# Optimization experiments

Hardware: AMD Instinct MI355X
Metric: run time of the kernel (lower is better)

The kernel has to match this reference:

```python
import jax, jax.numpy as jnp
import numpy as np
import math

HEAD_DIM = 128
DEPTH = 12
LAMBDA_INIT = 0.8 - 0.6 * math.exp(-0.3 * DEPTH)
EPS = 1e-5
SCALE = 1.0 / math.sqrt(HEAD_DIM / 2)


def setup_inputs() -> dict:
    key = jax.random.key(0)
    ks = jax.random.split(key, 8)
    b, t, d = 2, 4096, 2048
    return {
        "x": jax.random.normal(ks[0], (b, t, d), dtype=jnp.float32),
        "wq": jax.random.normal(ks[1], (d, HEAD_DIM), dtype=jnp.float32) * 0.02,
        "wk": jax.random.normal(ks[2], (d, HEAD_DIM), dtype=jnp.float32) * 0.02,
        "wv": jax.random.normal(ks[3], (d, HEAD_DIM), dtype=jnp.float32) * 0.02,
        "lambda_q1": jax.random.normal(ks[4], (HEAD_DIM // 2,), dtype=jnp.float32) * 0.1,
        "lambda_q2": jax.random.normal(ks[5], (HEAD_DIM // 2,), dtype=jnp.float32) * 0.1,
        "lambda_k1": jax.random.normal(ks[6], (HEAD_DIM // 2,), dtype=jnp.float32) * 0.1,
        "lambda_k2": jax.random.normal(ks[7], (HEAD_DIM // 2,), dtype=jnp.float32) * 0.1,
        "ln_weight": jnp.ones((HEAD_DIM,), dtype=jnp.float32),
    }


def reference(x, wq, wk, wv, lambda_q1, lambda_q2, lambda_k1, lambda_k2, ln_weight):
    b, t, d = x.shape
    q = x @ wq  # [b,t,hd]
    k = x @ wk
    v = x @ wv
    h = HEAD_DIM // 2
    q1, q2 = q[..., :h], q[..., h:]
    k1, k2 = k[..., :h], k[..., h:]
    # causal mask: True where attention is disallowed (strictly upper triangle)
    causal = jnp.triu(jnp.ones((t, t), dtype=bool), k=1)
    neg_inf = jnp.float32(-jnp.inf)

    def masked_softmax(qh, kh):
        scores = jnp.einsum('btd,bsd->bts', qh, kh) * SCALE
        scores = jnp.where(causal, neg_inf, scores)
        return jax.nn.softmax(scores, axis=-1)

    a1 = masked_softmax(q1, k1)
    a2 = masked_softmax(q2, k2)
    lmbda = (jnp.exp(jnp.sum(lambda_q1 * lambda_k1))
             - jnp.exp(jnp.sum(lambda_q2 * lambda_k2))
             + LAMBDA_INIT)
    diffattn = jnp.einsum('bts,bsd->btd', a1 - lmbda * a2, v)
    rms = jnp.sqrt(jnp.mean(diffattn * diffattn, axis=-1, keepdims=True) + EPS)
    out = (1.0 - LAMBDA_INIT) * (diffattn / rms * ln_weight)
    return out
```

## Files before the change

kernel.cpp:

```cpp
#include <hip/hip_runtime.h>
#include <stdint.h>

#define T_SEQ 4096
#define NB 2
#define D_MODEL 2048
#define HD 128

typedef __attribute__((ext_vector_type(4)))  float f32x4;
typedef __attribute__((ext_vector_type(16))) float f32x16;
typedef __attribute__((ext_vector_type(8)))  short bf16x8;
typedef __attribute__((ext_vector_type(4)))  unsigned u32x4;

#define LAMBDA_INIT 0.7836057665316244f
#define OUT_SCALE   0.21639423346837556f

__device__ __forceinline__ unsigned short f2bf(float f) {
  unsigned int u = __float_as_uint(f);
  u += 0x7FFFu + ((u >> 16) & 1u);
  return (unsigned short)(u >> 16);
}
__device__ __forceinline__ float bf2f(unsigned short h) {
  return __uint_as_float(((unsigned int)h) << 16);
}
__device__ __forceinline__ unsigned cvt_pk_bf16(float a, float b) {
  unsigned r;
  asm("v_cvt_pk_bf16_f32 %0, %1, %2" : "=v"(r) : "v"(a), "v"(b));
  return r;
}
__device__ __forceinline__ void gload16(const void* g, void* l) {
  __builtin_amdgcn_global_load_lds(
      (const __attribute__((address_space(1))) unsigned int*)g,
      (__attribute__((address_space(3))) unsigned int*)l, 16, 0, 0);
}

__global__ __launch_bounds__(256) void wtrans(
    const float* __restrict__ wq, const float* __restrict__ wk,
    const float* __restrict__ wv, unsigned short* __restrict__ wT)
{
  const int which = blockIdx.y;
  const int s = blockIdx.x;
  const float* w = (which == 0) ? wq : ((which == 1) ? wk : wv);
  const float scale = (which == 0) ? 0.125f : 1.0f;
  const int tid = threadIdx.x;
  #pragma unroll
  for (int j = 0; j < 4; ++j) {
    int cell = j * 256 + tid;
    int q = cell >> 7, n = cell & 127;
    int kb = s * 64 + q * 8;
    float v[8];
    #pragma unroll
    for (int e = 0; e < 8; ++e) v[e] = w[(size_t)(kb + e) * HD + n] * scale;
    u32x4 pk = { cvt_pk_bf16(v[0], v[1]), cvt_pk_bf16(v[2], v[3]),
                 cvt_pk_bf16(v[4], v[5]), cvt_pk_bf16(v[6], v[7]) };
    *reinterpret_cast<u32x4*>(&wT[(size_t)(which * 32 + s) * 8192 + (size_t)cell * 8]) = pk;
  }
}

__global__ __launch_bounds__(256, 2) void qkv_proj(
    const float* __restrict__ x, const unsigned short* __restrict__ wT,
    unsigned short* __restrict__ qb, unsigned short* __restrict__ kS,
    unsigned short* __restrict__ vS)
{
  __shared__ __align__(16) unsigned short Ab[2][4096];
  __shared__ __align__(16) unsigned short Bb[2][8192];
  const int which = blockIdx.y;
  const int m0 = blockIdx.x * 64;
  const int tid = threadIdx.x;
  const int lane = tid & 63, wid = tid >> 6;
  const int wm = wid >> 1, wn = wid & 1;
  const int fr = lane & 15, fq = lane >> 4;

  const unsigned short* wslab = wT + (size_t)which * 32 * 8192;

  const int arow = tid & 31, aq = tid >> 5;
  const float* xa = x + (size_t)(m0 + arow) * D_MODEL + aq * 8;
  const float* xb = xa + (size_t)32 * D_MODEL;

  f32x4 acc[2][4];
  #pragma unroll
  for (int i = 0; i < 2; ++i)
    #pragma unroll
    for (int j = 0; j < 4; ++j) acc[i][j] = (f32x4){0.f, 0.f, 0.f, 0.f};

  {
    f32x4 u0 = *reinterpret_cast<const f32x4*>(xa);
    f32x4 u1 = *reinterpret_cast<const f32x4*>(xa + 4);
    f32x4 u2 = *reinterpret_cast<const f32x4*>(xb);
    f32x4 u3 = *reinterpret_cast<const f32x4*>(xb + 4);
    u32x4 c0 = { cvt_pk_bf16(u0[0], u0[1]), cvt_pk_bf16(u0[2], u0[3]),
                 cvt_pk_bf16(u1[0], u1[1]), cvt_pk_bf16(u1[2], u1[3]) };
    u32x4 c1 = { cvt_pk_bf16(u2[0], u2[1]), cvt_pk_bf16(u2[2], u2[3]),
                 cvt_pk_bf16(u3[0], u3[1]), cvt_pk_bf16(u3[2], u3[3]) };
    *reinterpret_cast<u32x4*>(&Ab[0][(size_t)(aq * 64 + arow) * 8]) = c0;
    *reinterpret_cast<u32x4*>(&Ab[0][(size_t)(aq * 64 + arow + 32) * 8]) = c1;
    #pragma unroll
    for (int j = 0; j < 4; ++j) {
      int ch = wid * 4 + j;
      gload16(wslab + (size_t)ch * 512 + (size_t)lane * 8, (char*)&Bb[0][ch * 512]);
    }
  }
  f32x4 a0 = *reinterpret_cast<const f32x4*>(xa + 64);
  f32x4 a1 = *reinterpret_cast<const f32x4*>(xa + 68);
  f32x4 a2 = *reinterpret_cast<const f32x4*>(xb + 64);
  f32x4 a3 = *reinterpret_cast<const f32x4*>(xb + 68);
  __syncthreads();

  for (int it = 0; it < 32; ++it) {
    const int cur = it & 1;
    if (it < 31) {
      #pragma unroll
      for (int j = 0; j < 4; ++j) {
        int ch = wid * 4 + j;
        gload16(wslab + (size_t)(it + 1) * 8192 + (size_t)ch * 512 + (size_t)lane * 8,
                (char*)&Bb[cur ^ 1][ch * 512]);
      }
      u32x4 c0 = { cvt_pk_bf16(a0[0], a0[1]), cvt_pk_bf16(a0[2], a0[3]),
                   cvt_pk_bf16(a1[0], a1[1]), cvt_pk_bf16(a1[2], a1[3]) };
      u32x4 c1 = { cvt_pk_bf16(a2[0], a2[1]), cvt_pk_bf16(a2[2], a2[3]),
                   cvt_pk_bf16(a3[0], a3[1]), cvt_pk_bf16(a3[2], a3[3]) };
      *reinterpret_cast<u32x4*>(&Ab[cur ^ 1][(size_t)(aq * 64 + arow) * 8]) = c0;
      *reinterpret_cast<u32x4*>(&Ab[cur ^ 1][(size_t)(aq * 64 + arow + 32) * 8]) = c1;
      if (it < 30) {
        const int kn = (it + 2) * 64;
        a0 = *reinterpret_cast<const f32x4*>(xa + kn);
        a1 = *reinterpret_cast<const f32x4*>(xa + kn + 4);
        a2 = *reinterpret_cast<const f32x4*>(xb + kn);
        a3 = *reinterpret_cast<const f32x4*>(xb + kn + 4);
      }
    }
    bf16x8 ah[2][2], bh[2][4];
    #pragma unroll
    for (int mi = 0; mi < 2; ++mi) {
      int row = wm * 32 + mi * 16 + fr;
      ah[mi][0] = *reinterpret_cast<bf16x8*>(&Ab[cur][(size_t)(fq * 64 + row) * 8]);
      ah[mi][1] = *reinterpret_cast<bf16x8*>(&Ab[cur][(size_t)((4 + fq) * 64 + row) * 8]);
    }
    #pragma unroll
    for (int ni = 0; ni < 4; ++ni) {
      int nrow = wn * 64 + ni * 16 + fr;
      bh[0][ni] = *reinterpret_cast<bf16x8*>(&Bb[cur][(size_t)(fq * 128 + nrow) * 8]);
      bh[1][ni] = *reinterpret_cast<bf16x8*>(&Bb[cur][(size_t)((4 + fq) * 128 + nrow) * 8]);
    }
    #pragma unroll
    for (int kk = 0; kk < 2; ++kk)
      #pragma unroll
      for (int mi = 0; mi < 2; ++mi)
        #pragma unroll
        for (int ni = 0; ni < 4; ++ni)
          acc[mi][ni] = __builtin_amdgcn_mfma_f32_16x16x32_bf16(ah[mi][kk], bh[kk][ni], acc[mi][ni], 0, 0, 0);
    __syncthreads();
  }
  #pragma unroll
  for (int mi = 0; mi < 2; ++mi)
    #pragma unroll
    for (int ni = 0; ni < 4; ++ni) {
      int n = wn * 64 + ni * 16 + fr;
      #pragma unroll
      for (int r = 0; r < 4; ++r) {
        int m = m0 + wm * 32 + mi * 16 + fq * 4 + r;
        float vv = acc[mi][ni][r];
        int bb = m >> 12, tt = m & 4095;
        int kt = tt >> 5, kvl = tt & 31;
        if (which == 0) {
          qb[(size_t)m * HD + n] = f2bf(vv);
        } else if (which == 1) {
          int g = n >> 6, hl = n & 63;
          int ks = hl >> 4, r8 = (hl >> 3) & 1, e = hl & 7;
          size_t idx = ((((((size_t)bb * 128 + kt) * 2 + g) * 4) + ks) << 9)
                     + (size_t)(kvl + 32 * r8) * 8 + e;
          kS[idx] = f2bf(vv);
        } else {
          int f = kvl >> 4, r8 = (kvl >> 3) & 1, e = kvl & 7;
          int vcb = n >> 5;
          size_t idx = (((((size_t)bb * 128 + kt) * 8) + vcb * 2 + f) << 9)
                     + (size_t)((n & 31) + 32 * r8) * 8 + e;
          vS[idx] = f2bf(vv);
        }
      }
    }
}

template<int LOG2S>
__global__ __launch_bounds__(256, 2) void diff_attn_part(
    const unsigned short* __restrict__ qb, const unsigned short* __restrict__ kS,
    const unsigned short* __restrict__ vS,
    unsigned short* __restrict__ po, float* __restrict__ pm, float* __restrict__ pl)
{
  constexpr int S = 1 << LOG2S;
  const int tid = threadIdx.x, lane = tid & 63, wid = tid >> 6;
  const int wave_id = blockIdx.x * 4 + wid;
  const int sp = wave_id & (S - 1);
  const int g  = (wave_id >> LOG2S) & 1;
  const int qt_raw = (wave_id >> (LOG2S + 1)) & 127;
  const int b  = wave_id >> (LOG2S + 8);
  const int qt = 127 - qt_raw;
  const int slot = (((b * 128 + qt) * 2 + g) << LOG2S) + sp;
  const int lq = lane & 31, lh = lane >> 5;
  const int q0 = qt * 32;
  const int n  = qt + 1;
  const int kt0 = (n * sp) >> LOG2S;
  const int kt1 = (n * (sp + 1)) >> LOG2S;

  bf16x8 qf[4];
  const unsigned short* qp = qb + ((size_t)b * T_SEQ + q0 + lq) * HD + g * 64 + lh * 8;
  #pragma unroll
  for (int ks = 0; ks < 4; ++ks) qf[ks] = *reinterpret_cast<const bf16x8*>(qp + ks * 16);

  f32x16 acc[4];
  #pragma unroll
  for (int v = 0; v < 4; ++v)
    #pragma unroll
    for (int r = 0; r < 16; ++r) acc[v][r] = 0.f;
  float mrun = -1e30f, lrun = 0.f;

  const unsigned short* kbase = kS + ((size_t)(b * 128) * 2 + g) * 4 * 512 + lane * 8;
  const unsigned short* vbase = vS + (size_t)(b * 128) * 8 * 512 + lane * 8;
  #define KFRAG(kt, ks) (kbase + ((size_t)(kt) * 8 + (ks)) * 512)
  #define VFRAG(kt, f)  (vbase + ((size_t)(kt) * 8 + (f)) * 512)

  bf16x8 kf[4];
  if (kt0 < kt1) {
    #pragma unroll
    for (int ks = 0; ks < 4; ++ks)
      kf[ks] = *reinterpret_cast<const bf16x8*>(KFRAG(kt0, ks));
  }

  for (int kt = kt0; kt < kt1; ++kt) {
    bf16x8 vfa[4], vfb[4];
    #pragma unroll
    for (int vcb = 0; vcb < 4; ++vcb) {
      vfa[vcb] = *reinterpret_cast<const bf16x8*>(VFRAG(kt, vcb * 2));
      vfb[vcb] = *reinterpret_cast<const bf16x8*>(VFRAG(kt, vcb * 2 + 1));
    }
    bf16x8 kfn[4];
    const bool more = (kt + 1 < kt1);
    if (more) {
      #pragma unroll
      for (int ks = 0; ks < 4; ++ks)
        kfn[ks] = *reinterpret_cast<const bf16x8*>(KFRAG(kt + 1, ks));
    }
    f32x16 sc;
    #pragma unroll
    for (int r = 0; r < 16; ++r) sc[r] = 0.f;
    #pragma unroll
    for (int ks = 0; ks < 4; ++ks)
      sc = __builtin_amdgcn_mfma_f32_32x32x16_bf16(kf[ks], qf[ks], sc, 0, 0, 0);

    float p[16];
    if (kt == n - 1) {
      #pragma unroll
      for (int r = 0; r < 16; ++r) {
        int rloc = (r & 3) + 8 * (r >> 2) + 4 * lh;
        p[r] = (rloc > lq) ? -1e30f : sc[r];
      }
    } else {
      #pragma unroll
      for (int r = 0; r < 16; ++r) p[r] = sc[r];
    }
    float t16[16];
    #pragma unroll
    for (int r = 0; r < 16; ++r) t16[r] = p[r];
    #pragma unroll
    for (int st = 8; st >= 1; st >>= 1)
      #pragma unroll
      for (int r = 0; r < 8; ++r)
        if (r < st) t16[r] = fmaxf(t16[r], t16[r + st]);
    float pmax = fmaxf(t16[0], __shfl_xor(t16[0], 32));
    if (__any(pmax > mrun + 8.f)) {
      float mn = fmaxf(mrun, pmax);
      float al = __expf(mrun - mn);
      lrun *= al;
      #pragma unroll
      for (int v = 0; v < 4; ++v)
        #pragma unroll
        for (int r = 0; r < 16; ++r) acc[v][r] *= al;
      mrun = mn;
    }
    float psum;
    {
      float s16[16];
      #pragma unroll
      for (int r = 0; r < 16; ++r) { p[r] = __expf(p[r] - mrun); s16[r] = p[r]; }
      #pragma unroll
      for (int st = 8; st >= 1; st >>= 1)
        #pragma unroll
        for (int r = 0; r < 8; ++r)
          if (r < st) s16[r] += s16[r + st];
      psum = s16[0];
    }
    lrun += psum + __shfl_xor(psum, 32);

    unsigned A0 = cvt_pk_bf16(p[0],  p[1]),  A1 = cvt_pk_bf16(p[2],  p[3]);
    unsigned A2 = cvt_pk_bf16(p[4],  p[5]),  A3 = cvt_pk_bf16(p[6],  p[7]);
    unsigned A4 = cvt_pk_bf16(p[8],  p[9]),  A5 = cvt_pk_bf16(p[10], p[11]);
    unsigned A6 = cvt_pk_bf16(p[12], p[13]), A7 = cvt_pk_bf16(p[14], p[15]);
    unsigned pA0 = (unsigned)__shfl_xor((int)A0, 32);
    unsigned pA1 = (unsigned)__shfl_xor((int)A1, 32);
    unsigned pA2 = (unsigned)__shfl_xor((int)A2, 32);
    unsigned pA3 = (unsigned)__shfl_xor((int)A3, 32);
    unsigned pA4 = (unsigned)__shfl_xor((int)A4, 32);
    unsigned pA5 = (unsigned)__shfl_xor((int)A5, 32);
    unsigned pA6 = (unsigned)__shfl_xor((int)A6, 32);
    unsigned pA7 = (unsigned)__shfl_xor((int)A7, 32);
    u32x4 w0, w1;
    w0[0] = lh ? pA2 : A0;  w0[1] = lh ? pA3 : A1;
    w0[2] = lh ? A2  : pA0; w0[3] = lh ? A3  : pA1;
    w1[0] = lh ? pA6 : A4;  w1[1] = lh ? pA7 : A5;
    w1[2] = lh ? A6  : pA4; w1[3] = lh ? A7  : pA5;
    bf16x8 pb0 = *reinterpret_cast<bf16x8*>(&w0);
    bf16x8 pb1 = *reinterpret_cast<bf16x8*>(&w1);
    #pragma unroll
    for (int vcb = 0; vcb < 4; ++vcb) {
      acc[vcb] = __builtin_amdgcn_mfma_f32_32x32x16_bf16(vfa[vcb], pb0, acc[vcb], 0, 0, 0);
      acc[vcb] = __builtin_amdgcn_mfma_f32_32x32x16_bf16(vfb[vcb], pb1, acc[vcb], 0, 0, 0);
    }
    if (more) {
      #pragma unroll
      for (int ks = 0; ks < 4; ++ks) kf[ks] = kfn[ks];
    }
  }
  #undef KFRAG
  #undef VFRAG
  const size_t pbase = (size_t)slot * (HD * 32);
  #pragma unroll
  for (int vcb = 0; vcb < 4; ++vcb)
    #pragma unroll
    for (int r = 0; r < 16; ++r) {
      int vc = vcb * 32 + (r & 3) + 8 * (r >> 2) + 4 * lh;
      po[pbase + (size_t)vc * 32 + lq] = f2bf(acc[vcb][r]);
    }
  if (lane < 32) {
    pm[slot * 32 + lq] = mrun;
    pl[slot * 32 + lq] = lrun;
  }
}

template<int LOG2S>
__global__ __launch_bounds__(256) void diff_merge(
    const unsigned short* __restrict__ po, const float* __restrict__ pm,
    const float* __restrict__ pl,
    const float* __restrict__ lq1, const float* __restrict__ lq2,
    const float* __restrict__ lk1, const float* __restrict__ lk2,
    const float* __restrict__ lnw, float* __restrict__ out)
{
  constexpr int S = 1 << LOG2S;
  __shared__ float red[4][32];
  const int tid = threadIdx.x, lane = tid & 63, wid = tid >> 6;
  const int q = tid & 31, vg = tid >> 5;
  const int bq = blockIdx.x;
  const int b = bq >> 7, qt = bq & 127;

  float la = lq1[lane] * lk1[lane];
  float lb = lq2[lane] * lk2[lane];
  #pragma unroll
  for (int off = 32; off >= 1; off >>= 1) {
    la += __shfl_xor(la, off);
    lb += __shfl_xor(lb, off);
  }
  const float lam = __expf(la) - __expf(lb) + LAMBDA_INIT;

  const int p1 = (bq * 2 + 0) * S;
  const int p2 = (bq * 2 + 1) * S;
  float w1[S], w2[S];
  {
    float ms[S];
    #pragma unroll
    for (int s = 0; s < S; ++s) ms[s] = pm[(p1 + s) * 32 + q];
    float M = ms[0];
    #pragma unroll
    for (int s = 1; s < S; ++s) M = fmaxf(M, ms[s]);
    float L = 0.f;
    #pragma unroll
    for (int s = 0; s < S; ++s) { w1[s] = __expf(ms[s] - M); L += w1[s] * pl[(p1 + s) * 32 + q]; }
    float inv = 1.f / L;
    #pragma unroll
    for (int s = 0; s < S; ++s) w1[s] *= inv;
  }
  {
    float ms[S];
    #pragma unroll
    for (int s = 0; s < S; ++s) ms[s] = pm[(p2 + s) * 32 + q];
    float M = ms[0];
    #pragma unroll
    for (int s = 1; s < S; ++s) M = fmaxf(M, ms[s]);
    float L = 0.f;
    #pragma unroll
    for (int s = 0; s < S; ++s) { w2[s] = __expf(ms[s] - M); L += w2[s] * pl[(p2 + s) * 32 + q]; }
    float inv = lam / L;
    #pragma unroll
    for (int s = 0; s < S; ++s) w2[s] *= inv;
  }
  float d[16], ss = 0.f;
  #pragma unroll
  for (int i = 0; i < 16; ++i) {
    int vc = vg * 16 + i;
    float a1 = 0.f, a2 = 0.f;
    #pragma unroll
    for (int s = 0; s < S; ++s) {
      a1 += w1[s] * bf2f(po[(size_t)(p1 + s) * (HD * 32) + (size_t)vc * 32 + q]);
      a2 += w2[s] * bf2f(po[(size_t)(p2 + s) * (HD * 32) + (size_t)vc * 32 + q]);
    }
    d[i] = a1 - a2;
    ss += d[i] * d[i];
  }
  ss += __shfl_xor(ss, 32);
  if (lane < 32) red[wid][q] = ss;
  __syncthreads();
  float tot = red[0][q] + red[1][q] + red[2][q] + red[3][q];
  float rinv = 1.f / sqrtf(tot * (1.0f / HD) + 1e-5f);
  float* op = out + ((size_t)b * T_SEQ + qt * 32 + q) * HD + vg * 16;
  #pragma unroll
  for (int i = 0; i < 16; ++i) op[i] = OUT_SCALE * d[i] * rinv * lnw[vg * 16 + i];
}

extern "C" void kernel_launch(void* const* d_in, const int* in_sizes, int n_in,
                              void* d_out, int out_size, void* d_ws, size_t ws_size,
                              hipStream_t stream) {
  const float* x   = (const float*)d_in[0];
  const float* wq  = (const float*)d_in[1];
  const float* wk  = (const float*)d_in[2];
  const float* wv  = (const float*)d_in[3];
  const float* lq1 = (const float*)d_in[4];
  const float* lq2 = (const float*)d_in[5];
  const float* lk1 = (const float*)d_in[6];
  const float* lk2 = (const float*)d_in[7];
  const float* lnw = (const float*)d_in[8];
  float* out = (float*)d_out;

  const size_t N = (size_t)NB * T_SEQ * HD;
  const size_t WTN = (size_t)3 * 32 * 8192;
  int log2S = 3;
  for (; log2S > 0; --log2S) {
    size_t parts = ((size_t)NB * 128 * 2) << log2S;
    size_t need = 3 * N * 2 + WTN * 2 + parts * (HD * 32) * 2 + parts * 32 * 8;
    if (need <= ws_size) break;
  }
  const size_t parts = ((size_t)NB * 128 * 2) << log2S;

  unsigned short* qb = (unsigned short*)d_ws;
  unsigned short* kS = qb + N;
  unsigned short* vS = kS + N;
  unsigned short* wT = vS + N;
  unsigned short* po = wT + WTN;
  float* pm = (float*)(po + parts * (HD * 32));
  float* pl = pm + parts * 32;

  wtrans<<<dim3(32, 3), 256, 0, stream>>>(wq, wk, wv, wT);
  qkv_proj<<<dim3(128, 3), 256, 0, stream>>>(x, wT, qb, kS, vS);
  const int ablocks = (int)(parts / 4);
  switch (log2S) {
    case 3:
      diff_attn_part<3><<<dim3(ablocks), 256, 0, stream>>>(qb, kS, vS, po, pm, pl);
      diff_merge<3><<<dim3(NB * 128), 256, 0, stream>>>(po, pm, pl, lq1, lq2, lk1, lk2, lnw, out);
      break;
    case 2:
      diff_attn_part<2><<<dim3(ablocks), 256, 0, stream>>>(qb, kS, vS, po, pm, pl);
      diff_merge<2><<<dim3(NB * 128), 256, 0, stream>>>(po, pm, pl, lq1, lq2, lk1, lk2, lnw, out);
      break;
    case 1:
      diff_attn_part<1><<<dim3(ablocks), 256, 0, stream>>>(qb, kS, vS, po, pm, pl);
      diff_merge<1><<<dim3(NB * 128), 256, 0, stream>>>(po, pm, pl, lq1, lq2, lk1, lk2, lnw, out);
      break;
    default:
      diff_attn_part<0><<<dim3(ablocks), 256, 0, stream>>>(qb, kS, vS, po, pm, pl);
      diff_merge<0><<<dim3(NB * 128), 256, 0, stream>>>(po, pm, pl, lq1, lq2, lk1, lk2, lnw, out);
      break;
  }
}
```

Baseline: 97.90 us.

## Triple-buffer weight slabs in qkv_proj with explicit waitcnt-driven pipeline

Rewrites the QKV projection main loop so weight slabs are triple-buffered in LDS and prefetched two iterations ahead. The x register loads are double-buffered, with one barrier per iteration. Explicit s_waitcnt vmcnt values and sched_barriers replace the compiler's conservative waits so memory latency overlaps the MFMA work. The extra Bb buffer raises LDS use per block, which may affect occupancy at two blocks per CU. The hand-counted vmcnt values are fragile if the compiler reorders or adds memory operations.

```diff
diff --git a/kernel.cpp b/kernel.cpp
--- a/kernel.cpp
+++ b/kernel.cpp
@@ -62,7 +62,7 @@
     unsigned short* __restrict__ vS)
 {
   __shared__ __align__(16) unsigned short Ab[2][4096];
-  __shared__ __align__(16) unsigned short Bb[2][8192];
+  __shared__ __align__(16) unsigned short Bb[3][8192];
   const int which = blockIdx.y;
   const int m0 = blockIdx.x * 64;
   const int tid = threadIdx.x;
@@ -71,7 +71,6 @@
   const int fr = lane & 15, fq = lane >> 4;
 
   const unsigned short* wslab = wT + (size_t)which * 32 * 8192;
-
   const int arow = tid & 31, aq = tid >> 5;
   const float* xa = x + (size_t)(m0 + arow) * D_MODEL + aq * 8;
   const float* xb = xa + (size_t)32 * D_MODEL;
@@ -82,74 +81,95 @@
     #pragma unroll
     for (int j = 0; j < 4; ++j) acc[i][j] = (f32x4){0.f, 0.f, 0.f, 0.f};
 
-  {
-    f32x4 u0 = *reinterpret_cast<const f32x4*>(xa);
-    f32x4 u1 = *reinterpret_cast<const f32x4*>(xa + 4);
-    f32x4 u2 = *reinterpret_cast<const f32x4*>(xb);
-    f32x4 u3 = *reinterpret_cast<const f32x4*>(xb + 4);
-    u32x4 c0 = { cvt_pk_bf16(u0[0], u0[1]), cvt_pk_bf16(u0[2], u0[3]),
-                 cvt_pk_bf16(u1[0], u1[1]), cvt_pk_bf16(u1[2], u1[3]) };
-    u32x4 c1 = { cvt_pk_bf16(u2[0], u2[1]), cvt_pk_bf16(u2[2], u2[3]),
-                 cvt_pk_bf16(u3[0], u3[1]), cvt_pk_bf16(u3[2], u3[3]) };
-    *reinterpret_cast<u32x4*>(&Ab[0][(size_t)(aq * 64 + arow) * 8]) = c0;
-    *reinterpret_cast<u32x4*>(&Ab[0][(size_t)(aq * 64 + arow + 32) * 8]) = c1;
-    #pragma unroll
-    for (int j = 0; j < 4; ++j) {
-      int ch = wid * 4 + j;
-      gload16(wslab + (size_t)ch * 512 + (size_t)lane * 8, (char*)&Bb[0][ch * 512]);
-    }
-  }
-  f32x4 a0 = *reinterpret_cast<const f32x4*>(xa + 64);
-  f32x4 a1 = *reinterpret_cast<const f32x4*>(xa + 68);
-  f32x4 a2 = *reinterpret_cast<const f32x4*>(xb + 64);
-  f32x4 a3 = *reinterpret_cast<const f32x4*>(xb + 68);
-  __syncthreads();
-
-  for (int it = 0; it < 32; ++it) {
-    const int cur = it & 1;
-    if (it < 31) {
-      #pragma unroll
-      for (int j = 0; j < 4; ++j) {
-        int ch = wid * 4 + j;
-        gload16(wslab + (size_t)(it + 1) * 8192 + (size_t)ch * 512 + (size_t)lane * 8,
-                (char*)&Bb[cur ^ 1][ch * 512]);
-      }
-      u32x4 c0 = { cvt_pk_bf16(a0[0], a0[1]), cvt_pk_bf16(a0[2], a0[3]),
-                   cvt_pk_bf16(a1[0], a1[1]), cvt_pk_bf16(a1[2], a1[3]) };
-      u32x4 c1 = { cvt_pk_bf16(a2[0], a2[1]), cvt_pk_bf16(a2[2], a2[3]),
-                   cvt_pk_bf16(a3[0], a3[1]), cvt_pk_bf16(a3[2], a3[3]) };
-      *reinterpret_cast<u32x4*>(&Ab[cur ^ 1][(size_t)(aq * 64 + arow) * 8]) = c0;
-      *reinterpret_cast<u32x4*>(&Ab[cur ^ 1][(size_t)(aq * 64 + arow + 32) * 8]) = c1;
-      if (it < 30) {
-        const int kn = (it + 2) * 64;
-        a0 = *reinterpret_cast<const f32x4*>(xa + kn);
-        a1 = *reinterpret_cast<const f32x4*>(xa + kn + 4);
-        a2 = *reinterpret_cast<const f32x4*>(xb + kn);
-        a3 = *reinterpret_cast<const f32x4*>(xb + kn + 4);
-      }
-    }
-    bf16x8 ah[2][2], bh[2][4];
-    #pragma unroll
-    for (int mi = 0; mi < 2; ++mi) {
-      int row = wm * 32 + mi * 16 + fr;
-      ah[mi][0] = *reinterpret_cast<bf16x8*>(&Ab[cur][(size_t)(fq * 64 + row) * 8]);
-      ah[mi][1] = *reinterpret_cast<bf16x8*>(&Ab[cur][(size_t)((4 + fq) * 64 + row) * 8]);
-    }
-    #pragma unroll
-    for (int ni = 0; ni < 4; ++ni) {
-      int nrow = wn * 64 + ni * 16 + fr;
-      bh[0][ni] = *reinterpret_cast<bf16x8*>(&Bb[cur][(size_t)(fq * 128 + nrow) * 8]);
-      bh[1][ni] = *reinterpret_cast<bf16x8*>(&Bb[cur][(size_t)((4 + fq) * 128 + nrow) * 8]);
-    }
-    #pragma unroll
-    for (int kk = 0; kk < 2; ++kk)
-      #pragma unroll
-      for (int mi = 0; mi < 2; ++mi)
-        #pragma unroll
-        for (int ni = 0; ni < 4; ++ni)
-          acc[mi][ni] = __builtin_amdgcn_mfma_f32_16x16x32_bf16(ah[mi][kk], bh[kk][ni], acc[mi][ni], 0, 0, 0);
-    __syncthreads();
-  }
+  f32x4 rA0[4], rA1[4];
+
+#define ALOAD(dst, slab) do {                                              \
+    const int kn_ = (slab) * 64;                                           \
+    dst[0] = *reinterpret_cast<const f32x4*>(xa + kn_);                    \
+    dst[1] = *reinterpret_cast<const f32x4*>(xa + kn_ + 4);                \
+    dst[2] = *reinterpret_cast<const f32x4*>(xb + kn_);                    \
+    dst[3] = *reinterpret_cast<const f32x4*>(xb + kn_ + 4);                \
+  } while (0)
+
+#define AWRITE(src, slab) do {                                             \
+    unsigned short* ab_ = &Ab[(slab) & 1][0];                              \
+    u32x4 c0_ = { cvt_pk_bf16(src[0][0], src[0][1]),                       \
+                  cvt_pk_bf16(src[0][2], src[0][3]),                       \
+                  cvt_pk_bf16(src[1][0], src[1][1]),                       \
+                  cvt_pk_bf16(src[1][2], src[1][3]) };                     \
+    u32x4 c1_ = { cvt_pk_bf16(src[2][0], src[2][1]),                       \
+                  cvt_pk_bf16(src[2][2], src[2][3]),                       \
+                  cvt_pk_bf16(src[3][0], src[3][1]),                       \
+                  cvt_pk_bf16(src[3][2], src[3][3]) };                     \
+    *reinterpret_cast<u32x4*>(ab_ + (size_t)(aq * 64 + arow) * 8) = c0_;   \
+    *reinterpret_cast<u32x4*>(ab_ + (size_t)(aq * 64 + arow + 32) * 8) = c1_; \
+  } while (0)
+
+#define BDMA(slab) do {                                                    \
+    unsigned short* bb_ = &Bb[(slab) % 3][0] + (wid * 4) * 512;            \
+    const unsigned short* gs_ = wslab + (size_t)(slab) * 8192              \
+                              + (size_t)(wid * 4) * 512 + (size_t)lane * 8;\
+    gload16(gs_,        (char*)(bb_));                                     \
+    gload16(gs_ + 512,  (char*)(bb_ + 512));                               \
+    gload16(gs_ + 1024, (char*)(bb_ + 1024));                              \
+    gload16(gs_ + 1536, (char*)(bb_ + 1536));                              \
+  } while (0)
+
+  ALOAD(rA0, 0);
+  __builtin_amdgcn_sched_barrier(0);
+  BDMA(0);
+  __builtin_amdgcn_sched_barrier(0);
+  BDMA(1);
+  __builtin_amdgcn_sched_barrier(0);
+  ALOAD(rA1, 1);
+  __builtin_amdgcn_sched_barrier(0);
+  AWRITE(rA0, 0);
+
+#define QITER(t, WSRC, LDST) do {                                          \
+    if ((t) == 0)      asm volatile("s_waitcnt vmcnt(8) lgkmcnt(0)" ::: "memory");  \
+    else if ((t) < 31) asm volatile("s_waitcnt vmcnt(12) lgkmcnt(0)" ::: "memory"); \
+    else               asm volatile("s_waitcnt vmcnt(4) lgkmcnt(0)" ::: "memory");  \
+    __builtin_amdgcn_s_barrier();                                          \
+    __builtin_amdgcn_sched_barrier(0);                                     \
+    if ((t) + 2 < 32) BDMA((t) + 2);                                       \
+    __builtin_amdgcn_sched_barrier(0);                                     \
+    if ((t) + 1 < 32) AWRITE(WSRC, (t) + 1);                               \
+    if ((t) + 2 < 32) ALOAD(LDST, (t) + 2);                                \
+    __builtin_amdgcn_sched_barrier(0);                                     \
+    const unsigned short* bc_ = &Bb[(t) % 3][0];                           \
+    const unsigned short* ac_ = &Ab[(t) & 1][0];                           \
+    bf16x8 ah_[2][2], bh_[2][4];                                           \
+    _Pragma("unroll")                                                      \
+    for (int mi = 0; mi < 2; ++mi) {                                       \
+      int row = wm * 32 + mi * 16 + fr;                                    \
+      ah_[mi][0] = *reinterpret_cast<const bf16x8*>(ac_ + (size_t)(fq * 64 + row) * 8);        \
+      ah_[mi][1] = *reinterpret_cast<const bf16x8*>(ac_ + (size_t)((4 + fq) * 64 + row) * 8);  \
+    }                                                                      \
+    _Pragma("unroll")                                                      \
+    for (int ni = 0; ni < 4; ++ni) {                                       \
+      int nrow = wn * 64 + ni * 16 + fr;                                   \
+      bh_[0][ni] = *reinterpret_cast<const bf16x8*>(bc_ + (size_t)(fq * 128 + nrow) * 8);      \
+      bh_[1][ni] = *reinterpret_cast<const bf16x8*>(bc_ + (size_t)((4 + fq) * 128 + nrow) * 8);\
+    }                                                                      \
+    _Pragma("unroll")                                                      \
+    for (int kk = 0; kk < 2; ++kk)                                         \
+      _Pragma("unroll")                                                    \
+      for (int mi = 0; mi < 2; ++mi)                                       \
+        _Pragma("unroll")                                                  \
+        for (int ni = 0; ni < 4; ++ni)                                     \
+          acc[mi][ni] = __builtin_amdgcn_mfma_f32_16x16x32_bf16(ah_[mi][kk], bh_[kk][ni], acc[mi][ni], 0, 0, 0); \
+  } while (0)
+
+  #pragma unroll 1
+  for (int th = 0; th < 16; ++th) {
+    QITER(2 * th,     rA1, rA0);
+    QITER(2 * th + 1, rA0, rA1);
+  }
+#undef QITER
+#undef BDMA
+#undef AWRITE
+#undef ALOAD
+
   #pragma unroll
   for (int mi = 0; mi < 2; ++mi)
     #pragma unroll
```

Measured after the change: 90.43 us. 7.6% less time.

## Rewrite QKV projection to stream operands directly into registers without LDS

Applied to the files above, without the earlier changes.

The QKV projection GEMM drops LDS staging and block-wide barriers. Each wave now loads its 32 rows of x and the pre-transposed bf16 weight fragments straight from global memory into registers and converts x to bf16 in registers. Loads are software-pipelined two k-steps ahead. Each block covers 128 rows, which halves the grid, and each wave computes the full 128-column output. This removes LDS traffic and __syncthreads, but weight fragments are no longer shared across waves, which raises global/L2 load volume and register pressure and lowers block count.

```diff
diff --git a/kernel.cpp b/kernel.cpp
--- a/kernel.cpp
+++ b/kernel.cpp
@@ -26,11 +26,6 @@
   unsigned r;
   asm("v_cvt_pk_bf16_f32 %0, %1, %2" : "=v"(r) : "v"(a), "v"(b));
   return r;
-}
-__device__ __forceinline__ void gload16(const void* g, void* l) {
-  __builtin_amdgcn_global_load_lds(
-      (const __attribute__((address_space(1))) unsigned int*)g,
-      (__attribute__((address_space(3))) unsigned int*)l, 16, 0, 0);
 }
 
 __global__ __launch_bounds__(256) void wtrans(
@@ -56,109 +51,100 @@
   }
 }
 
-__global__ __launch_bounds__(256, 2) void qkv_proj(
+__global__ __launch_bounds__(256) void qkv_proj(
     const float* __restrict__ x, const unsigned short* __restrict__ wT,
     unsigned short* __restrict__ qb, unsigned short* __restrict__ kS,
     unsigned short* __restrict__ vS)
 {
-  __shared__ __align__(16) unsigned short Ab[2][4096];
-  __shared__ __align__(16) unsigned short Bb[2][8192];
   const int which = blockIdx.y;
-  const int m0 = blockIdx.x * 64;
   const int tid = threadIdx.x;
   const int lane = tid & 63, wid = tid >> 6;
-  const int wm = wid >> 1, wn = wid & 1;
   const int fr = lane & 15, fq = lane >> 4;
-
-  const unsigned short* wslab = wT + (size_t)which * 32 * 8192;
-
-  const int arow = tid & 31, aq = tid >> 5;
-  const float* xa = x + (size_t)(m0 + arow) * D_MODEL + aq * 8;
-  const float* xb = xa + (size_t)32 * D_MODEL;
-
-  f32x4 acc[2][4];
-  #pragma unroll
-  for (int i = 0; i < 2; ++i)
-    #pragma unroll
-    for (int j = 0; j < 4; ++j) acc[i][j] = (f32x4){0.f, 0.f, 0.f, 0.f};
-
-  {
-    f32x4 u0 = *reinterpret_cast<const f32x4*>(xa);
-    f32x4 u1 = *reinterpret_cast<const f32x4*>(xa + 4);
-    f32x4 u2 = *reinterpret_cast<const f32x4*>(xb);
-    f32x4 u3 = *reinterpret_cast<const f32x4*>(xb + 4);
-    u32x4 c0 = { cvt_pk_bf16(u0[0], u0[1]), cvt_pk_bf16(u0[2], u0[3]),
-                 cvt_pk_bf16(u1[0], u1[1]), cvt_pk_bf16(u1[2], u1[3]) };
-    u32x4 c1 = { cvt_pk_bf16(u2[0], u2[1]), cvt_pk_bf16(u2[2], u2[3]),
-                 cvt_pk_bf16(u3[0], u3[1]), cvt_pk_bf16(u3[2], u3[3]) };
-    *reinterpret_cast<u32x4*>(&Ab[0][(size_t)(aq * 64 + arow) * 8]) = c0;
-    *reinterpret_cast<u32x4*>(&Ab[0][(size_t)(aq * 64 + arow + 32) * 8]) = c1;
-    #pragma unroll
-    for (int j = 0; j < 4; ++j) {
-      int ch = wid * 4 + j;
-      gload16(wslab + (size_t)ch * 512 + (size_t)lane * 8, (char*)&Bb[0][ch * 512]);
-    }
-  }
-  f32x4 a0 = *reinterpret_cast<const f32x4*>(xa + 64);
-  f32x4 a1 = *reinterpret_cast<const f32x4*>(xa + 68);
-  f32x4 a2 = *reinterpret_cast<const f32x4*>(xb + 64);
-  f32x4 a3 = *reinterpret_cast<const f32x4*>(xb + 68);
-  __syncthreads();
-
-  for (int it = 0; it < 32; ++it) {
-    const int cur = it & 1;
-    if (it < 31) {
-      #pragma unroll
-      for (int j = 0; j < 4; ++j) {
-        int ch = wid * 4 + j;
-        gload16(wslab + (size_t)(it + 1) * 8192 + (size_t)ch * 512 + (size_t)lane * 8,
-                (char*)&Bb[cur ^ 1][ch * 512]);
-      }
-      u32x4 c0 = { cvt_pk_bf16(a0[0], a0[1]), cvt_pk_bf16(a0[2], a0[3]),
-                   cvt_pk_bf16(a1[0], a1[1]), cvt_pk_bf16(a1[2], a1[3]) };
-      u32x4 c1 = { cvt_pk_bf16(a2[0], a2[1]), cvt_pk_bf16(a2[2], a2[3]),
-                   cvt_pk_bf16(a3[0], a3[1]), cvt_pk_bf16(a3[2], a3[3]) };
-      *reinterpret_cast<u32x4*>(&Ab[cur ^ 1][(size_t)(aq * 64 + arow) * 8]) = c0;
-      *reinterpret_cast<u32x4*>(&Ab[cur ^ 1][(size_t)(aq * 64 + arow + 32) * 8]) = c1;
-      if (it < 30) {
-        const int kn = (it + 2) * 64;
-        a0 = *reinterpret_cast<const f32x4*>(xa + kn);
-        a1 = *reinterpret_cast<const f32x4*>(xa + kn + 4);
-        a2 = *reinterpret_cast<const f32x4*>(xb + kn);
-        a3 = *reinterpret_cast<const f32x4*>(xb + kn + 4);
-      }
-    }
-    bf16x8 ah[2][2], bh[2][4];
-    #pragma unroll
-    for (int mi = 0; mi < 2; ++mi) {
-      int row = wm * 32 + mi * 16 + fr;
-      ah[mi][0] = *reinterpret_cast<bf16x8*>(&Ab[cur][(size_t)(fq * 64 + row) * 8]);
-      ah[mi][1] = *reinterpret_cast<bf16x8*>(&Ab[cur][(size_t)((4 + fq) * 64 + row) * 8]);
-    }
-    #pragma unroll
-    for (int ni = 0; ni < 4; ++ni) {
-      int nrow = wn * 64 + ni * 16 + fr;
-      bh[0][ni] = *reinterpret_cast<bf16x8*>(&Bb[cur][(size_t)(fq * 128 + nrow) * 8]);
-      bh[1][ni] = *reinterpret_cast<bf16x8*>(&Bb[cur][(size_t)((4 + fq) * 128 + nrow) * 8]);
-    }
-    #pragma unroll
-    for (int kk = 0; kk < 2; ++kk)
-      #pragma unroll
-      for (int mi = 0; mi < 2; ++mi)
-        #pragma unroll
-        for (int ni = 0; ni < 4; ++ni)
-          acc[mi][ni] = __builtin_amdgcn_mfma_f32_16x16x32_bf16(ah[mi][kk], bh[kk][ni], acc[mi][ni], 0, 0, 0);
-    __syncthreads();
-  }
+  const int m0w = blockIdx.x * 128 + wid * 32;
+
+  const float* xa = x + (size_t)(m0w + fr) * D_MODEL;
+  const float* xb = xa + (size_t)16 * D_MODEL;
+  const unsigned short* wbase = wT + (size_t)which * 32 * 8192 + (size_t)fr * 8;
+
+  f32x4 acc0[8], acc1[8];
+  #pragma unroll
+  for (int j = 0; j < 8; ++j) {
+    acc0[j] = (f32x4){0.f, 0.f, 0.f, 0.f};
+    acc1[j] = (f32x4){0.f, 0.f, 0.f, 0.f};
+  }
+
+  f32x4 X[2][4], Y[2][4];
+  bf16x8 B0[8], B1[8];
+
+#define AISSUE(S, c) do {                                                  \
+    const int k0_ = (c) * 64 + fq * 8;                                     \
+    S[0][0] = *reinterpret_cast<const f32x4*>(xa + k0_);                   \
+    S[0][1] = *reinterpret_cast<const f32x4*>(xa + k0_ + 4);               \
+    S[0][2] = *reinterpret_cast<const f32x4*>(xb + k0_);                   \
+    S[0][3] = *reinterpret_cast<const f32x4*>(xb + k0_ + 4);               \
+    S[1][0] = *reinterpret_cast<const f32x4*>(xa + k0_ + 32);              \
+    S[1][1] = *reinterpret_cast<const f32x4*>(xa + k0_ + 36);              \
+    S[1][2] = *reinterpret_cast<const f32x4*>(xb + k0_ + 32);              \
+    S[1][3] = *reinterpret_cast<const f32x4*>(xb + k0_ + 36);              \
+  } while (0)
+
+#define BISSUE(Bc, t) do {                                                 \
+    const unsigned short* bp_ = wbase + (size_t)((t) >> 1) * 8192          \
+                              + (size_t)((((t) & 1) * 4 + fq) * 128) * 8;  \
+    _Pragma("unroll")                                                      \
+    for (int ni = 0; ni < 8; ++ni)                                         \
+      Bc[ni] = *reinterpret_cast<const bf16x8*>(bp_ + (size_t)ni * 128);   \
+  } while (0)
+
+#define QITER(S, j, Bc) do {                                               \
+    u32x4 ua_ = { cvt_pk_bf16(S[j][0][0], S[j][0][1]),                     \
+                  cvt_pk_bf16(S[j][0][2], S[j][0][3]),                     \
+                  cvt_pk_bf16(S[j][1][0], S[j][1][1]),                     \
+                  cvt_pk_bf16(S[j][1][2], S[j][1][3]) };                   \
+    u32x4 ub_ = { cvt_pk_bf16(S[j][2][0], S[j][2][1]),                     \
+                  cvt_pk_bf16(S[j][2][2], S[j][2][3]),                     \
+                  cvt_pk_bf16(S[j][3][0], S[j][3][1]),                     \
+                  cvt_pk_bf16(S[j][3][2], S[j][3][3]) };                   \
+    bf16x8 a0_ = *reinterpret_cast<bf16x8*>(&ua_);                         \
+    bf16x8 a1_ = *reinterpret_cast<bf16x8*>(&ub_);                         \
+    _Pragma("unroll")                                                      \
+    for (int ni = 0; ni < 8; ++ni) {                                       \
+      acc0[ni] = __builtin_amdgcn_mfma_f32_16x16x32_bf16(a0_, Bc[ni], acc0[ni], 0, 0, 0); \
+      acc1[ni] = __builtin_amdgcn_mfma_f32_16x16x32_bf16(a1_, Bc[ni], acc1[ni], 0, 0, 0); \
+    }                                                                      \
+  } while (0)
+
+  AISSUE(X, 0);
+  AISSUE(Y, 1);
+  BISSUE(B0, 0);
+  BISSUE(B1, 1);
+
+  for (int u = 0; u < 16; ++u) {
+    const int t0 = 4 * u;
+    QITER(X, 0, B0);
+    if (t0 + 2 < 64) BISSUE(B0, t0 + 2);
+    QITER(X, 1, B1);
+    if (t0 + 3 < 64) BISSUE(B1, t0 + 3);
+    if (u < 15) AISSUE(X, 2 * u + 2);
+    QITER(Y, 0, B0);
+    if (t0 + 4 < 64) BISSUE(B0, t0 + 4);
+    QITER(Y, 1, B1);
+    if (t0 + 5 < 64) BISSUE(B1, t0 + 5);
+    if (u < 15) AISSUE(Y, 2 * u + 3);
+  }
+#undef QITER
+#undef BISSUE
+#undef AISSUE
+
   #pragma unroll
   for (int mi = 0; mi < 2; ++mi)
     #pragma unroll
-    for (int ni = 0; ni < 4; ++ni) {
-      int n = wn * 64 + ni * 16 + fr;
+    for (int ni = 0; ni < 8; ++ni) {
+      int n = ni * 16 + fr;
       #pragma unroll
       for (int r = 0; r < 4; ++r) {
-        int m = m0 + wm * 32 + mi * 16 + fq * 4 + r;
-        float vv = acc[mi][ni][r];
+        int m = m0w + mi * 16 + fq * 4 + r;
+        float vv = mi ? acc1[ni][r] : acc0[ni][r];
         int bb = m >> 12, tt = m & 4095;
         int kt = tt >> 5, kvl = tt & 31;
         if (which == 0) {
@@ -446,7 +432,7 @@
   float* pl = pm + parts * 32;
 
   wtrans<<<dim3(32, 3), 256, 0, stream>>>(wq, wk, wv, wT);
-  qkv_proj<<<dim3(128, 3), 256, 0, stream>>>(x, wT, qb, kS, vS);
+  qkv_proj<<<dim3(64, 3), 256, 0, stream>>>(x, wT, qb, kS, vS);
   const int ablocks = (int)(parts / 4);
   switch (log2S) {
     case 3:
```

Result: slower. 103.1 us (+5.3%).
